# Performance work log

Measured on AMD Instinct MI355X. Metric: run time of the kernel, lower is better.

Reference implementation:

```python
import jax, jax.numpy as jnp
import numpy as np

N = 10000        # nodes
E = 640000       # edges (avg degree 64)
D_IN = 128       # input feature dim
H = 128          # hidden dim
B = 64           # graphs in batch


def setup_inputs() -> dict:
    key = jax.random.key(0)
    ks = jax.random.split(key, 12)
    x = jax.random.normal(ks[0], (N, D_IN), dtype=jnp.float32)
    edge_index = jax.random.randint(ks[1], (2, E), 0, N, dtype=jnp.int32)
    batch = jnp.sort(jax.random.randint(ks[2], (N,), 0, B, dtype=jnp.int32))
    def lin(k, fan_in, fan_out):
        s = 1.0 / np.sqrt(fan_in)
        kw, kb = jax.random.split(k)
        W = jax.random.uniform(kw, (fan_in, fan_out), jnp.float32, -s, s)
        b = jax.random.uniform(kb, (fan_out,), jnp.float32, -s, s)
        return W, b
    W1, b1 = lin(ks[3], D_IN, H)
    W2, b2 = lin(ks[4], H, H)
    W3, b3 = lin(ks[5], H, H)
    Wp, bp = lin(ks[6], H, 1)
    return {"x": x, "edge_index": edge_index, "batch": batch,
            "W1": W1, "b1": b1, "W2": W2, "b2": b2,
            "W3": W3, "b3": b3, "Wp": Wp, "bp": bp}


def reference(x, edge_index, batch, W1, b1, W2, b2, W3, b3, Wp, bp):
    # --- GCN normalization with self-loops (shared across layers; edge weights all 1) ---
    loop = jnp.arange(N, dtype=edge_index.dtype)
    src = jnp.concatenate([edge_index[0], loop])  # [E+N] message sources
    dst = jnp.concatenate([edge_index[1], loop])  # [E+N] message targets
    deg = jax.ops.segment_sum(jnp.ones_like(dst, dtype=x.dtype), dst, num_segments=N)
    dinv = jax.lax.rsqrt(jnp.maximum(deg, 1.0))   # deg >= 1 due to self-loops
    norm = dinv[src] * dinv[dst]                  # [E+N]

    def gcn_layer(h, W, b):
        h = h @ W                                             # [N, H] transform first
        msg = norm[:, None] * h[src]                          # [E+N, H] gathered messages
        return jax.ops.segment_sum(msg, dst, num_segments=N) + b

    h = jax.nn.relu(gcn_layer(x, W1, b1))   # dropout is identity in eval mode
    h = jax.nn.relu(gcn_layer(h, W2, b2))
    h = gcn_layer(h, W3, b3)

    # --- global mean pool over graphs ---
    sums = jax.ops.segment_sum(h, batch, num_segments=B)                       # [B, H]
    cnt = jax.ops.segment_sum(jnp.ones((N,), h.dtype), batch, num_segments=B)  # [B]
    emb = sums / jnp.maximum(cnt, 1.0)[:, None]

    return emb @ Wp + bp  # [B, 1]
```

## Files before the change

### kernel.cpp

```cpp
#include <hip/hip_runtime.h>

#define D 128
#define HS 10016
#define CSHIFT 13
#define CSZ (1 << CSHIFT)

__device__ __forceinline__ unsigned short f2bf(float f) {
  unsigned int u = __float_as_uint(f);
  return (unsigned short)((u + 0x7FFFu + ((u >> 16) & 1u)) >> 16);
}


__global__ __launch_bounds__(256) void k_hist(const int* __restrict__ ei, int E, int M,
                                              const int* __restrict__ batch,
                                              int* __restrict__ pk,
                                              unsigned short* __restrict__ rank16,
                                              int* __restrict__ g_hist,
                                              int* __restrict__ g_bh) {
  __shared__ int h[HS];
  __shared__ int bh[64];
  for (int j = threadIdx.x; j < HS; j += 256) h[j] = 0;
  if (threadIdx.x < 64) bh[threadIdx.x] = 0;
  __syncthreads();
  int w = blockIdx.x;
  int i0 = w << CSHIFT;
  int i1 = i0 + CSZ; if (i1 > M) i1 = M;
  for (int i = i0 + threadIdx.x; i < i1; i += 256) {
    int s, d;
    if (i < E) { s = ei[i]; d = ei[E + i]; }
    else { s = i - E; d = s; atomicAdd(&bh[batch[s]], 1); }
    pk[i] = s | (d << 14);
    int r = atomicAdd(&h[d], 1);
    rank16[i] = (unsigned short)r;
  }
  __syncthreads();
  for (int j = threadIdx.x; j < HS; j += 256) g_hist[w * HS + j] = h[j];
  if (threadIdx.x < 64) g_bh[blockIdx.x * 64 + threadIdx.x] = bh[threadIdx.x];
}

__global__ __launch_bounds__(256) void k_merge(int* __restrict__ g_hist,
                                               const int* __restrict__ g_bh,
                                               int* cnt, float* dinv,
                                               int* cntB, float* accB,
                                               int N, int B, int HW) {
  int j = blockIdx.x * 256 + threadIdx.x;
  if (j < N) {
    int run = 0;
    for (int w = 0; w < HW; ++w) {
      int idx = w * HS + j;
      int t = g_hist[idx];
      g_hist[idx] = run;
      run += t;
    }
    cnt[j] = run;
    dinv[j] = rsqrtf((float)run);
  }
  if (j < B) {
    int c = 0;
    for (int w = 0; w < HW; ++w) c += g_bh[w * 64 + j];
    cntB[j] = c;
    accB[j] = 0.f;
  }
}

__global__ __launch_bounds__(1024) void k_scan(const int* __restrict__ cnt,
                                               int* offs, int N) {
  __shared__ int wsum[16];
  __shared__ int carry_s;
  int tid = threadIdx.x, wid = tid >> 6, lane = tid & 63;
  if (tid == 0) carry_s = 0;
  __syncthreads();
  for (int base = 0; base < N; base += 1024) {
    int i = base + tid;
    int v = (i < N) ? cnt[i] : 0;
    int x = v;
    #pragma unroll
    for (int s = 1; s < 64; s <<= 1) {
      int t = __shfl_up(x, s);
      if (lane >= s) x += t;
    }
    if (lane == 63) wsum[wid] = x;
    __syncthreads();
    int woff = 0;
    for (int w = 0; w < wid; ++w) woff += wsum[w];
    int carry = carry_s;
    if (i < N) offs[i] = carry + woff + x - v;
    __syncthreads();
    if (tid == 1023) carry_s = carry + woff + x;
  }
  __syncthreads();
  if (tid == 0) offs[N] = carry_s;
}

__global__ __launch_bounds__(256) void k_fill(const int* __restrict__ pk,
                                              const unsigned short* __restrict__ rank16,
                                              const int* __restrict__ colpre,
                                              const int* __restrict__ offs,
                                              const float* __restrict__ dinv,
                                              float2* __restrict__ epair, int M, int N) {
  int part = blockIdx.x & 7;
  int j    = blockIdx.x >> 3;
  int nj   = gridDim.x >> 3;
  int lo = (int)((long long)part * N >> 3);
  int hi = (int)((long long)(part + 1) * N >> 3);
  for (int i = j * 256 + threadIdx.x; i < M; i += nj * 256) {
    int rec = pk[i];
    int d = rec >> 14;
    if (d < lo || d >= hi) continue;
    int s = rec & 0x3FFF;
    int w = i >> CSHIFT;
    int pos = offs[d] + colpre[w * HS + d] + (int)rank16[i];
    epair[pos] = make_float2(__int_as_float(s), dinv[s] * dinv[d]);
  }
}

__global__ __launch_bounds__(256) void k_gemm(const float* __restrict__ A,
                                              const float* __restrict__ W,
                                              unsigned short* __restrict__ C, int N) {
  __shared__ float As[32][36];
  __shared__ float Ws[32][128];
  int tid = threadIdx.x;
  int tx = tid & 31;
  int ty = tid >> 5;
  int r0 = blockIdx.x * 32;
  float acc[4][4] = {};

  for (int k0 = 0; k0 < 128; k0 += 32) {
    for (int i = tid; i < 1024; i += 256) {
      int kk = i >> 5, j4 = i & 31;
      float4 w = *(const float4*)(W + (size_t)(k0 + kk) * 128 + j4 * 4);
      *(float4*)(&Ws[kk][j4 * 4]) = w;
    }
    {
      int r = tid >> 3, k4 = tid & 7;
      int row = r0 + r;
      float4 a = make_float4(0.f, 0.f, 0.f, 0.f);
      if (row < N) a = *(const float4*)(A + (size_t)row * 128 + k0 + k4 * 4);
      As[k4 * 4 + 0][r] = a.x;
      As[k4 * 4 + 1][r] = a.y;
      As[k4 * 4 + 2][r] = a.z;
      As[k4 * 4 + 3][r] = a.w;
    }
    __syncthreads();
    #pragma unroll
    for (int k = 0; k < 32; ++k) {
      float4 a = *(const float4*)(&As[k][ty * 4]);
      float4 b = *(const float4*)(&Ws[k][tx * 4]);
      float av[4] = {a.x, a.y, a.z, a.w};
      float bv[4] = {b.x, b.y, b.z, b.w};
      #pragma unroll
      for (int i = 0; i < 4; ++i)
        #pragma unroll
        for (int j = 0; j < 4; ++j)
          acc[i][j] = fmaf(av[i], bv[j], acc[i][j]);
    }
    __syncthreads();
  }
  #pragma unroll
  for (int i = 0; i < 4; ++i) {
    int row = r0 + ty * 4 + i;
    if (row < N) {
      ushort4 o;
      o.x = f2bf(acc[i][0]); o.y = f2bf(acc[i][1]);
      o.z = f2bf(acc[i][2]); o.w = f2bf(acc[i][3]);
      *(ushort4*)(C + (size_t)row * 128 + tx * 4) = o;
    }
  }
}

__device__ __forceinline__ void agg_core(const unsigned short* __restrict__ t,
                                         const float2* __restrict__ epair,
                                         int beg, int end, int lane,
                                         float* acc) {
  int half = lane >> 5;
  int q = lane & 31;
  const unsigned short* tq = t + (q << 2);

  int e = beg;
  for (; e + 16 <= end; e += 16) {
    float2 ep[16];
    #pragma unroll
    for (int u = 0; u < 16; ++u) ep[u] = epair[e + u];
    uint2 v[8];
    #pragma unroll
    for (int u = 0; u < 8; ++u) {
      int s0 = __float_as_int(ep[2 * u].x);
      int s1 = __float_as_int(ep[2 * u + 1].x);
      int s = half ? s1 : s0;
      v[u] = *(const uint2*)(tq + ((size_t)s << 7));
    }
    #pragma unroll
    for (int u = 0; u < 8; ++u) {
      float w = half ? ep[2 * u + 1].y : ep[2 * u].y;
      acc[0] = fmaf(w, __uint_as_float(v[u].x << 16), acc[0]);
      acc[1] = fmaf(w, __uint_as_float(v[u].x & 0xFFFF0000u), acc[1]);
      acc[2] = fmaf(w, __uint_as_float(v[u].y << 16), acc[2]);
      acc[3] = fmaf(w, __uint_as_float(v[u].y & 0xFFFF0000u), acc[3]);
    }
  }
  if (e < end) {
    float2 ep[16];
    #pragma unroll
    for (int u = 0; u < 16; ++u) {
      int idx = (e + u < end) ? (e + u) : (end - 1);
      ep[u] = epair[idx];
      if (e + u >= end) ep[u].y = 0.f;
    }
    uint2 v[8];
    #pragma unroll
    for (int u = 0; u < 8; ++u) {
      int s0 = __float_as_int(ep[2 * u].x);
      int s1 = __float_as_int(ep[2 * u + 1].x);
      int s = half ? s1 : s0;
      v[u] = *(const uint2*)(tq + ((size_t)s << 7));
    }
    #pragma unroll
    for (int u = 0; u < 8; ++u) {
      float w = half ? ep[2 * u + 1].y : ep[2 * u].y;
      acc[0] = fmaf(w, __uint_as_float(v[u].x << 16), acc[0]);
      acc[1] = fmaf(w, __uint_as_float(v[u].x & 0xFFFF0000u), acc[1]);
      acc[2] = fmaf(w, __uint_as_float(v[u].y << 16), acc[2]);
      acc[3] = fmaf(w, __uint_as_float(v[u].y & 0xFFFF0000u), acc[3]);
    }
  }
  #pragma unroll
  for (int j = 0; j < 4; ++j) acc[j] += __shfl_xor(acc[j], 32);
}

__global__ __launch_bounds__(256, 4) void k_agg(const unsigned short* __restrict__ t,
                                                const float2* __restrict__ epair,
                                                const int* __restrict__ offs,
                                                const float* __restrict__ bias,
                                                float* __restrict__ hout, int N, int relu) {
  int node = __builtin_amdgcn_readfirstlane(blockIdx.x * 4 + (threadIdx.x >> 6));
  int lane = threadIdx.x & 63;
  if (node >= N) return;
  int beg = offs[node], end = offs[node + 1];
  float acc[4] = {0.f, 0.f, 0.f, 0.f};
  agg_core(t, epair, beg, end, lane, acc);
  int q = lane & 31;
  float4 bb = *(const float4*)(bias + (q << 2));
  float o0 = acc[0] + bb.x, o1 = acc[1] + bb.y, o2 = acc[2] + bb.z, o3 = acc[3] + bb.w;
  if (relu) {
    o0 = fmaxf(o0, 0.f); o1 = fmaxf(o1, 0.f);
    o2 = fmaxf(o2, 0.f); o3 = fmaxf(o3, 0.f);
  }
  if (lane < 32)
    *(float4*)(hout + (size_t)node * 128 + (q << 2)) = make_float4(o0, o1, o2, o3);
}

__global__ __launch_bounds__(256, 4) void k_agg_pool(const unsigned short* __restrict__ t,
                                                     const float2* __restrict__ epair,
                                                     const int* __restrict__ offs,
                                                     const float* __restrict__ bias,
                                                     const float* __restrict__ Wp,
                                                     const int* __restrict__ batch,
                                                     float* accB, int N) {
  int node = __builtin_amdgcn_readfirstlane(blockIdx.x * 4 + (threadIdx.x >> 6));
  int lane = threadIdx.x & 63;
  if (node >= N) return;
  int beg = offs[node], end = offs[node + 1];
  float acc[4] = {0.f, 0.f, 0.f, 0.f};
  agg_core(t, epair, beg, end, lane, acc);
  int q = lane & 31;
  float4 bb = *(const float4*)(bias + (q << 2));
  float4 wv = *(const float4*)(Wp + (q << 2));
  float p = (acc[0] + bb.x) * wv.x + (acc[1] + bb.y) * wv.y +
            (acc[2] + bb.z) * wv.z + (acc[3] + bb.w) * wv.w;
  #pragma unroll
  for (int s = 16; s; s >>= 1) p += __shfl_xor(p, s);
  if (lane == 0) atomicAdd(&accB[batch[node]], p);
}

__global__ __launch_bounds__(64) void k_final(const float* __restrict__ accB,
                                              const int* __restrict__ cntB,
                                              const float* __restrict__ bp,
                                              float* out, int B) {
  int b = blockIdx.x * 64 + threadIdx.x;
  if (b < B) {
    float c = (float)(cntB[b] > 1 ? cntB[b] : 1);
    out[b] = accB[b] / c + bp[0];
  }
}


extern "C" void kernel_launch(void* const* d_in, const int* in_sizes, int n_in,
                              void* d_out, int out_size, void* d_ws, size_t ws_size,
                              hipStream_t stream) {
  const float* x    = (const float*)d_in[0];
  const int*   ei   = (const int*)d_in[1];
  const int*   batch= (const int*)d_in[2];
  const float* W1   = (const float*)d_in[3];
  const float* b1   = (const float*)d_in[4];
  const float* W2   = (const float*)d_in[5];
  const float* b2   = (const float*)d_in[6];
  const float* W3   = (const float*)d_in[7];
  const float* b3   = (const float*)d_in[8];
  const float* Wp   = (const float*)d_in[9];
  const float* bp   = (const float*)d_in[10];
  float* out = (float*)d_out;

  int N = in_sizes[0] / D;
  int E = in_sizes[1] / 2;
  int B = out_size;
  int M = E + N;
  int HW = (M + CSZ - 1) >> CSHIFT;

  char* p = (char*)d_ws;
  float2* epair  = (float2*)p;          p += (size_t)M * 8;
  float* hbuf    = (float*)p;           p += (size_t)N * D * 4;
  unsigned short* tbuf = (unsigned short*)p; p += (size_t)N * D * 2;
  int*   pk      = (int*)p;             p += (size_t)M * 4;
  unsigned short* rank16 = (unsigned short*)p; p += (size_t)M * 2;
  int*   g_hist  = (int*)p;             p += (size_t)HW * HS * 4;
  int*   g_bh    = (int*)p;             p += (size_t)HW * 64 * 4;
  int*   cnt     = (int*)p;             p += (size_t)N * 4;
  int*   offs    = (int*)p;             p += (size_t)(N + 1) * 4;
  float* dinv    = (float*)p;           p += (size_t)N * 4;
  float* accB    = (float*)p;           p += (size_t)B * 4;
  int*   cntB    = (int*)p;             p += (size_t)B * 4;

  int gG  = (N + 31) / 32;
  int gA  = (N + 3) / 4;
  int gMg = (N + 255) / 256;

  k_hist <<<HW, 256, 0, stream>>>(ei, E, M, batch, pk, rank16, g_hist, g_bh);
  k_merge<<<gMg, 256, 0, stream>>>(g_hist, g_bh, cnt, dinv, cntB, accB, N, B, HW);
  k_scan <<<1, 1024, 0, stream>>>(cnt, offs, N);
  k_fill <<<4096, 256, 0, stream>>>(pk, rank16, g_hist, offs, dinv, epair, M, N);

  k_gemm<<<gG, 256, 0, stream>>>(x, W1, tbuf, N);
  k_agg <<<gA, 256, 0, stream>>>(tbuf, epair, offs, b1, hbuf, N, 1);
  k_gemm<<<gG, 256, 0, stream>>>(hbuf, W2, tbuf, N);
  k_agg <<<gA, 256, 0, stream>>>(tbuf, epair, offs, b2, hbuf, N, 1);
  k_gemm<<<gG, 256, 0, stream>>>(hbuf, W3, tbuf, N);
  k_agg_pool<<<gA, 256, 0, stream>>>(tbuf, epair, offs, b3, Wp, batch, accB, N);
  k_final<<<(B + 63) / 64, 64, 0, stream>>>(accB, cntB, bp, out, B);
}
```

Measured before the change: 291.7 us.

## Replace gather aggregation with source-side scatter into per-edge message buffer

Adds a second CSR keyed by source node, whose entries hold each edge's slot in the destination-sorted order. Each layer now writes normalized bf16 messages into a per-edge message buffer laid out in destination order (k_msg), then sums them contiguously per destination (k_sum). The aim is to replace random row gathers with sequential reads, paid for by random row scatter-writes plus a much larger intermediate buffer (M*256 bytes) and extra histogram, scan and fill work. The new path only runs when the workspace is large enough; otherwise the old gather path is kept.

```diff
diff --git a/kernel.cpp b/kernel.cpp
--- a/kernel.cpp
+++ b/kernel.cpp
@@ -8,6 +8,296 @@
 __device__ __forceinline__ unsigned short f2bf(float f) {
   unsigned int u = __float_as_uint(f);
   return (unsigned short)((u + 0x7FFFu + ((u >> 16) & 1u)) >> 16);
+}
+
+
+__global__ __launch_bounds__(1024) void k_scan(const int* __restrict__ cnt,
+                                               int* offs, int N) {
+  __shared__ int wsum[16];
+  __shared__ int carry_s;
+  int tid = threadIdx.x, wid = tid >> 6, lane = tid & 63;
+  if (tid == 0) carry_s = 0;
+  __syncthreads();
+  for (int base = 0; base < N; base += 1024) {
+    int i = base + tid;
+    int v = (i < N) ? cnt[i] : 0;
+    int x = v;
+    #pragma unroll
+    for (int s = 1; s < 64; s <<= 1) {
+      int t = __shfl_up(x, s);
+      if (lane >= s) x += t;
+    }
+    if (lane == 63) wsum[wid] = x;
+    __syncthreads();
+    int woff = 0;
+    for (int w = 0; w < wid; ++w) woff += wsum[w];
+    int carry = carry_s;
+    if (i < N) offs[i] = carry + woff + x - v;
+    __syncthreads();
+    if (tid == 1023) carry_s = carry + woff + x;
+  }
+  __syncthreads();
+  if (tid == 0) offs[N] = carry_s;
+}
+
+__global__ __launch_bounds__(256) void k_gemm(const float* __restrict__ A,
+                                              const float* __restrict__ W,
+                                              unsigned short* __restrict__ C, int N) {
+  __shared__ float As[32][36];
+  __shared__ float Ws[32][128];
+  int tid = threadIdx.x;
+  int tx = tid & 31;
+  int ty = tid >> 5;
+  int r0 = blockIdx.x * 32;
+  float acc[4][4] = {};
+
+  for (int k0 = 0; k0 < 128; k0 += 32) {
+    for (int i = tid; i < 1024; i += 256) {
+      int kk = i >> 5, j4 = i & 31;
+      float4 w = *(const float4*)(W + (size_t)(k0 + kk) * 128 + j4 * 4);
+      *(float4*)(&Ws[kk][j4 * 4]) = w;
+    }
+    {
+      int r = tid >> 3, k4 = tid & 7;
+      int row = r0 + r;
+      float4 a = make_float4(0.f, 0.f, 0.f, 0.f);
+      if (row < N) a = *(const float4*)(A + (size_t)row * 128 + k0 + k4 * 4);
+      As[k4 * 4 + 0][r] = a.x;
+      As[k4 * 4 + 1][r] = a.y;
+      As[k4 * 4 + 2][r] = a.z;
+      As[k4 * 4 + 3][r] = a.w;
+    }
+    __syncthreads();
+    #pragma unroll
+    for (int k = 0; k < 32; ++k) {
+      float4 a = *(const float4*)(&As[k][ty * 4]);
+      float4 b = *(const float4*)(&Ws[k][tx * 4]);
+      float av[4] = {a.x, a.y, a.z, a.w};
+      float bv[4] = {b.x, b.y, b.z, b.w};
+      #pragma unroll
+      for (int i = 0; i < 4; ++i)
+        #pragma unroll
+        for (int j = 0; j < 4; ++j)
+          acc[i][j] = fmaf(av[i], bv[j], acc[i][j]);
+    }
+    __syncthreads();
+  }
+  #pragma unroll
+  for (int i = 0; i < 4; ++i) {
+    int row = r0 + ty * 4 + i;
+    if (row < N) {
+      ushort4 o;
+      o.x = f2bf(acc[i][0]); o.y = f2bf(acc[i][1]);
+      o.z = f2bf(acc[i][2]); o.w = f2bf(acc[i][3]);
+      *(ushort4*)(C + (size_t)row * 128 + tx * 4) = o;
+    }
+  }
+}
+
+__global__ __launch_bounds__(64) void k_final(const float* __restrict__ accB,
+                                              const int* __restrict__ cntB,
+                                              const float* __restrict__ bp,
+                                              float* out, int B) {
+  int b = blockIdx.x * 64 + threadIdx.x;
+  if (b < B) {
+    float c = (float)(cntB[b] > 1 ? cntB[b] : 1);
+    out[b] = accB[b] / c + bp[0];
+  }
+}
+
+
+__global__ __launch_bounds__(256) void k_hist2(const int* __restrict__ ei, int E, int M,
+                                               const int* __restrict__ batch,
+                                               int* __restrict__ pk,
+                                               unsigned short* __restrict__ rank16,
+                                               unsigned short* __restrict__ srank16,
+                                               int* __restrict__ g_hist,
+                                               int* __restrict__ g_hist2,
+                                               int* __restrict__ g_bh) {
+  __shared__ int h[HS];
+  __shared__ int h2[HS];
+  __shared__ int bh[64];
+  for (int j = threadIdx.x; j < HS; j += 256) { h[j] = 0; h2[j] = 0; }
+  if (threadIdx.x < 64) bh[threadIdx.x] = 0;
+  __syncthreads();
+  int w = blockIdx.x;
+  int i0 = w << CSHIFT;
+  int i1 = i0 + CSZ; if (i1 > M) i1 = M;
+  for (int i = i0 + threadIdx.x; i < i1; i += 256) {
+    int s, d;
+    if (i < E) { s = ei[i]; d = ei[E + i]; }
+    else { s = i - E; d = s; atomicAdd(&bh[batch[s]], 1); }
+    pk[i] = s | (d << 14);
+    rank16[i]  = (unsigned short)atomicAdd(&h[d], 1);
+    srank16[i] = (unsigned short)atomicAdd(&h2[s], 1);
+  }
+  __syncthreads();
+  for (int j = threadIdx.x; j < HS; j += 256) {
+    g_hist[w * HS + j]  = h[j];
+    g_hist2[w * HS + j] = h2[j];
+  }
+  if (threadIdx.x < 64) g_bh[blockIdx.x * 64 + threadIdx.x] = bh[threadIdx.x];
+}
+
+__global__ __launch_bounds__(256) void k_merge2(int* __restrict__ g_hist,
+                                                int* __restrict__ g_hist2,
+                                                const int* __restrict__ g_bh,
+                                                int* cnt, int* scnt, float* dinv,
+                                                int* cntB, float* accB,
+                                                int N, int B, int HW) {
+  int j = blockIdx.x * 256 + threadIdx.x;
+  if (j < N) {
+    int run = 0;
+    for (int w = 0; w < HW; ++w) {
+      int idx = w * HS + j;
+      int t = g_hist[idx]; g_hist[idx] = run; run += t;
+    }
+    cnt[j] = run;
+    dinv[j] = rsqrtf((float)run);
+    int run2 = 0;
+    for (int w = 0; w < HW; ++w) {
+      int idx = w * HS + j;
+      int t = g_hist2[idx]; g_hist2[idx] = run2; run2 += t;
+    }
+    scnt[j] = run2;
+  }
+  if (j < B) {
+    int c = 0;
+    for (int w = 0; w < HW; ++w) c += g_bh[w * 64 + j];
+    cntB[j] = c;
+    accB[j] = 0.f;
+  }
+}
+
+__global__ __launch_bounds__(256) void k_fillS(const int* __restrict__ pk,
+                                               const unsigned short* __restrict__ rank16,
+                                               const unsigned short* __restrict__ srank16,
+                                               const int* __restrict__ dcolpre,
+                                               const int* __restrict__ scolpre,
+                                               const int* __restrict__ offs,
+                                               const int* __restrict__ soffs,
+                                               const float* __restrict__ dinv,
+                                               float2* __restrict__ scsr, int M, int N) {
+  int part = blockIdx.x & 7;
+  int j    = blockIdx.x >> 3;
+  int nj   = gridDim.x >> 3;
+  int lo = (int)((long long)part * N >> 3);
+  int hi = (int)((long long)(part + 1) * N >> 3);
+  for (int i = j * 256 + threadIdx.x; i < M; i += nj * 256) {
+    int rec = pk[i];
+    int s = rec & 0x3FFF;
+    if (s < lo || s >= hi) continue;
+    int d = rec >> 14;
+    int w = i >> CSHIFT;
+    int dpos = offs[d]  + dcolpre[w * HS + d] + (int)rank16[i];
+    int spos = soffs[s] + scolpre[w * HS + s] + (int)srank16[i];
+    scsr[spos] = make_float2(__int_as_float(dpos), dinv[s] * dinv[d]);
+  }
+}
+
+__global__ __launch_bounds__(256, 8) void k_msg(const unsigned short* __restrict__ t,
+                                                const float2* __restrict__ scsr,
+                                                const int* __restrict__ soffs,
+                                                unsigned short* __restrict__ msg, int N) {
+  int node = __builtin_amdgcn_readfirstlane(blockIdx.x * 4 + (threadIdx.x >> 6));
+  int lane = threadIdx.x & 63;
+  if (node >= N) return;
+  unsigned int rv = *(const unsigned int*)(t + ((size_t)node << 7) + (lane << 1));
+  float hx = __uint_as_float(rv << 16);
+  float hy = __uint_as_float(rv & 0xFFFF0000u);
+  int beg = soffs[node], end = soffs[node + 1];
+  int e = beg;
+#define EMIT(r) { \
+    int dpos = __float_as_int((r).x); float nw = (r).y; \
+    float a_ = nw * hx, b_ = nw * hy; unsigned int o_; \
+    asm("v_cvt_pk_bf16_f32 %0, %1, %2" : "=v"(o_) : "v"(a_), "v"(b_)); \
+    *(unsigned int*)(msg + ((size_t)dpos << 7) + (lane << 1)) = o_; }
+  for (; e + 4 <= end; e += 4) {
+    float2 r0 = scsr[e], r1 = scsr[e + 1], r2 = scsr[e + 2], r3 = scsr[e + 3];
+    EMIT(r0); EMIT(r1); EMIT(r2); EMIT(r3);
+  }
+  for (; e < end; ++e) { float2 r = scsr[e]; EMIT(r); }
+#undef EMIT
+}
+
+__device__ __forceinline__ void sum_core(const unsigned short* __restrict__ msg,
+                                         int beg, int end, int grp, int sub,
+                                         float* acc) {
+  int cn = end - beg;
+  int c = 0;
+  for (; c + 4 <= cn; c += 4) {
+    uint4 v = *(const uint4*)(msg + ((size_t)(beg + c + grp) << 7) + (sub << 3));
+    acc[0] += __uint_as_float(v.x << 16); acc[1] += __uint_as_float(v.x & 0xFFFF0000u);
+    acc[2] += __uint_as_float(v.y << 16); acc[3] += __uint_as_float(v.y & 0xFFFF0000u);
+    acc[4] += __uint_as_float(v.z << 16); acc[5] += __uint_as_float(v.z & 0xFFFF0000u);
+    acc[6] += __uint_as_float(v.w << 16); acc[7] += __uint_as_float(v.w & 0xFFFF0000u);
+  }
+  if (c < cn) {
+    int rem = cn - c;
+    int gi = grp < rem ? grp : rem - 1;
+    uint4 v = *(const uint4*)(msg + ((size_t)(beg + c + gi) << 7) + (sub << 3));
+    if (grp < rem) {
+      acc[0] += __uint_as_float(v.x << 16); acc[1] += __uint_as_float(v.x & 0xFFFF0000u);
+      acc[2] += __uint_as_float(v.y << 16); acc[3] += __uint_as_float(v.y & 0xFFFF0000u);
+      acc[4] += __uint_as_float(v.z << 16); acc[5] += __uint_as_float(v.z & 0xFFFF0000u);
+      acc[6] += __uint_as_float(v.w << 16); acc[7] += __uint_as_float(v.w & 0xFFFF0000u);
+    }
+  }
+  #pragma unroll
+  for (int j = 0; j < 8; ++j) {
+    acc[j] += __shfl_xor(acc[j], 16);
+    acc[j] += __shfl_xor(acc[j], 32);
+  }
+}
+
+__global__ __launch_bounds__(256, 8) void k_sum(const unsigned short* __restrict__ msg,
+                                                const int* __restrict__ offs,
+                                                const float* __restrict__ bias,
+                                                float* __restrict__ hout, int N, int relu) {
+  int node = blockIdx.x * 4 + (threadIdx.x >> 6);
+  int lane = threadIdx.x & 63;
+  if (node >= N) return;
+  int grp = lane >> 4, sub = lane & 15;
+  float acc[8] = {};
+  sum_core(msg, offs[node], offs[node + 1], grp, sub, acc);
+  if (lane < 16) {
+    float4 b0 = *(const float4*)(bias + (sub << 3));
+    float4 b1 = *(const float4*)(bias + (sub << 3) + 4);
+    float o[8] = {acc[0] + b0.x, acc[1] + b0.y, acc[2] + b0.z, acc[3] + b0.w,
+                  acc[4] + b1.x, acc[5] + b1.y, acc[6] + b1.z, acc[7] + b1.w};
+    if (relu) {
+      #pragma unroll
+      for (int j = 0; j < 8; ++j) o[j] = fmaxf(o[j], 0.f);
+    }
+    float* hp = hout + (size_t)node * 128 + (sub << 3);
+    *(float4*)hp       = make_float4(o[0], o[1], o[2], o[3]);
+    *(float4*)(hp + 4) = make_float4(o[4], o[5], o[6], o[7]);
+  }
+}
+
+__global__ __launch_bounds__(256, 8) void k_sum_pool(const unsigned short* __restrict__ msg,
+                                                     const int* __restrict__ offs,
+                                                     const float* __restrict__ bias,
+                                                     const float* __restrict__ Wp,
+                                                     const int* __restrict__ batch,
+                                                     float* accB, int N) {
+  int node = blockIdx.x * 4 + (threadIdx.x >> 6);
+  int lane = threadIdx.x & 63;
+  if (node >= N) return;
+  int grp = lane >> 4, sub = lane & 15;
+  float acc[8] = {};
+  sum_core(msg, offs[node], offs[node + 1], grp, sub, acc);
+  float4 b0 = *(const float4*)(bias + (sub << 3));
+  float4 b1 = *(const float4*)(bias + (sub << 3) + 4);
+  float4 w0 = *(const float4*)(Wp + (sub << 3));
+  float4 w1 = *(const float4*)(Wp + (sub << 3) + 4);
+  float p = (acc[0] + b0.x) * w0.x + (acc[1] + b0.y) * w0.y +
+            (acc[2] + b0.z) * w0.z + (acc[3] + b0.w) * w0.w +
+            (acc[4] + b1.x) * w1.x + (acc[5] + b1.y) * w1.y +
+            (acc[6] + b1.z) * w1.z + (acc[7] + b1.w) * w1.w;
+  #pragma unroll
+  for (int s = 1; s < 16; s <<= 1) p += __shfl_xor(p, s);
+  if (lane == 0) atomicAdd(&accB[batch[node]], p);
 }
 
 
@@ -30,8 +320,7 @@
     if (i < E) { s = ei[i]; d = ei[E + i]; }
     else { s = i - E; d = s; atomicAdd(&bh[batch[s]], 1); }
     pk[i] = s | (d << 14);
-    int r = atomicAdd(&h[d], 1);
-    rank16[i] = (unsigned short)r;
+    rank16[i] = (unsigned short)atomicAdd(&h[d], 1);
   }
   __syncthreads();
   for (int j = threadIdx.x; j < HS; j += 256) g_hist[w * HS + j] = h[j];
@@ -48,9 +337,7 @@
     int run = 0;
     for (int w = 0; w < HW; ++w) {
       int idx = w * HS + j;
-      int t = g_hist[idx];
-      g_hist[idx] = run;
-      run += t;
+      int t = g_hist[idx]; g_hist[idx] = run; run += t;
     }
     cnt[j] = run;
     dinv[j] = rsqrtf((float)run);
@@ -61,35 +348,6 @@
     cntB[j] = c;
     accB[j] = 0.f;
   }
-}
-
-__global__ __launch_bounds__(1024) void k_scan(const int* __restrict__ cnt,
-                                               int* offs, int N) {
-  __shared__ int wsum[16];
-  __shared__ int carry_s;
-  int tid = threadIdx.x, wid = tid >> 6, lane = tid & 63;
-  if (tid == 0) carry_s = 0;
-  __syncthreads();
-  for (int base = 0; base < N; base += 1024) {
-    int i = base + tid;
-    int v = (i < N) ? cnt[i] : 0;
-    int x = v;
-    #pragma unroll
-    for (int s = 1; s < 64; s <<= 1) {
-      int t = __shfl_up(x, s);
-      if (lane >= s) x += t;
-    }
-    if (lane == 63) wsum[wid] = x;
-    __syncthreads();
-    int woff = 0;
-    for (int w = 0; w < wid; ++w) woff += wsum[w];
-    int carry = carry_s;
-    if (i < N) offs[i] = carry + woff + x - v;
-    __syncthreads();
-    if (tid == 1023) carry_s = carry + woff + x;
-  }
-  __syncthreads();
-  if (tid == 0) offs[N] = carry_s;
 }
 
 __global__ __launch_bounds__(256) void k_fill(const int* __restrict__ pk,
@@ -114,60 +372,6 @@
   }
 }
 
-__global__ __launch_bounds__(256) void k_gemm(const float* __restrict__ A,
-                                              const float* __restrict__ W,
-                                              unsigned short* __restrict__ C, int N) {
-  __shared__ float As[32][36];
-  __shared__ float Ws[32][128];
-  int tid = threadIdx.x;
-  int tx = tid & 31;
-  int ty = tid >> 5;
-  int r0 = blockIdx.x * 32;
-  float acc[4][4] = {};
-
-  for (int k0 = 0; k0 < 128; k0 += 32) {
-    for (int i = tid; i < 1024; i += 256) {
-      int kk = i >> 5, j4 = i & 31;
-      float4 w = *(const float4*)(W + (size_t)(k0 + kk) * 128 + j4 * 4);
-      *(float4*)(&Ws[kk][j4 * 4]) = w;
-    }
-    {
-      int r = tid >> 3, k4 = tid & 7;
-      int row = r0 + r;
-      float4 a = make_float4(0.f, 0.f, 0.f, 0.f);
-      if (row < N) a = *(const float4*)(A + (size_t)row * 128 + k0 + k4 * 4);
-      As[k4 * 4 + 0][r] = a.x;
-      As[k4 * 4 + 1][r] = a.y;
-      As[k4 * 4 + 2][r] = a.z;
-      As[k4 * 4 + 3][r] = a.w;
-    }
-    __syncthreads();
-    #pragma unroll
-    for (int k = 0; k < 32; ++k) {
-      float4 a = *(const float4*)(&As[k][ty * 4]);
-      float4 b = *(const float4*)(&Ws[k][tx * 4]);
-      float av[4] = {a.x, a.y, a.z, a.w};
-      float bv[4] = {b.x, b.y, b.z, b.w};
-      #pragma unroll
-      for (int i = 0; i < 4; ++i)
-        #pragma unroll
-        for (int j = 0; j < 4; ++j)
-          acc[i][j] = fmaf(av[i], bv[j], acc[i][j]);
-    }
-    __syncthreads();
-  }
-  #pragma unroll
-  for (int i = 0; i < 4; ++i) {
-    int row = r0 + ty * 4 + i;
-    if (row < N) {
-      ushort4 o;
-      o.x = f2bf(acc[i][0]); o.y = f2bf(acc[i][1]);
-      o.z = f2bf(acc[i][2]); o.w = f2bf(acc[i][3]);
-      *(ushort4*)(C + (size_t)row * 128 + tx * 4) = o;
-    }
-  }
-}
-
 __device__ __forceinline__ void agg_core(const unsigned short* __restrict__ t,
                                          const float2* __restrict__ epair,
                                          int beg, int end, int lane,
@@ -175,7 +379,6 @@
   int half = lane >> 5;
   int q = lane & 31;
   const unsigned short* tq = t + (q << 2);
-
   int e = beg;
   for (; e + 16 <= end; e += 16) {
     float2 ep[16];
@@ -235,9 +438,8 @@
   int node = __builtin_amdgcn_readfirstlane(blockIdx.x * 4 + (threadIdx.x >> 6));
   int lane = threadIdx.x & 63;
   if (node >= N) return;
-  int beg = offs[node], end = offs[node + 1];
   float acc[4] = {0.f, 0.f, 0.f, 0.f};
-  agg_core(t, epair, beg, end, lane, acc);
+  agg_core(t, epair, offs[node], offs[node + 1], lane, acc);
   int q = lane & 31;
   float4 bb = *(const float4*)(bias + (q << 2));
   float o0 = acc[0] + bb.x, o1 = acc[1] + bb.y, o2 = acc[2] + bb.z, o3 = acc[3] + bb.w;
@@ -259,9 +461,8 @@
   int node = __builtin_amdgcn_readfirstlane(blockIdx.x * 4 + (threadIdx.x >> 6));
   int lane = threadIdx.x & 63;
   if (node >= N) return;
-  int beg = offs[node], end = offs[node + 1];
   float acc[4] = {0.f, 0.f, 0.f, 0.f};
-  agg_core(t, epair, beg, end, lane, acc);
+  agg_core(t, epair, offs[node], offs[node + 1], lane, acc);
   int q = lane & 31;
   float4 bb = *(const float4*)(bias + (q << 2));
   float4 wv = *(const float4*)(Wp + (q << 2));
@@ -270,17 +471,6 @@
   #pragma unroll
   for (int s = 16; s; s >>= 1) p += __shfl_xor(p, s);
   if (lane == 0) atomicAdd(&accB[batch[node]], p);
-}
-
-__global__ __launch_bounds__(64) void k_final(const float* __restrict__ accB,
-                                              const int* __restrict__ cntB,
-                                              const float* __restrict__ bp,
-                                              float* out, int B) {
-  int b = blockIdx.x * 64 + threadIdx.x;
-  if (b < B) {
-    float c = (float)(cntB[b] > 1 ? cntB[b] : 1);
-    out[b] = accB[b] / c + bp[0];
-  }
 }
 
 
@@ -306,34 +496,88 @@
   int M = E + N;
   int HW = (M + CSZ - 1) >> CSHIFT;
 
-  char* p = (char*)d_ws;
-  float2* epair  = (float2*)p;          p += (size_t)M * 8;
-  float* hbuf    = (float*)p;           p += (size_t)N * D * 4;
-  unsigned short* tbuf = (unsigned short*)p; p += (size_t)N * D * 2;
-  int*   pk      = (int*)p;             p += (size_t)M * 4;
-  unsigned short* rank16 = (unsigned short*)p; p += (size_t)M * 2;
-  int*   g_hist  = (int*)p;             p += (size_t)HW * HS * 4;
-  int*   g_bh    = (int*)p;             p += (size_t)HW * 64 * 4;
-  int*   cnt     = (int*)p;             p += (size_t)N * 4;
-  int*   offs    = (int*)p;             p += (size_t)(N + 1) * 4;
-  float* dinv    = (float*)p;           p += (size_t)N * 4;
-  float* accB    = (float*)p;           p += (size_t)B * 4;
-  int*   cntB    = (int*)p;             p += (size_t)B * 4;
-
   int gG  = (N + 31) / 32;
   int gA  = (N + 3) / 4;
   int gMg = (N + 255) / 256;
 
-  k_hist <<<HW, 256, 0, stream>>>(ei, E, M, batch, pk, rank16, g_hist, g_bh);
-  k_merge<<<gMg, 256, 0, stream>>>(g_hist, g_bh, cnt, dinv, cntB, accB, N, B, HW);
-  k_scan <<<1, 1024, 0, stream>>>(cnt, offs, N);
-  k_fill <<<4096, 256, 0, stream>>>(pk, rank16, g_hist, offs, dinv, epair, M, N);
-
-  k_gemm<<<gG, 256, 0, stream>>>(x, W1, tbuf, N);
-  k_agg <<<gA, 256, 0, stream>>>(tbuf, epair, offs, b1, hbuf, N, 1);
-  k_gemm<<<gG, 256, 0, stream>>>(hbuf, W2, tbuf, N);
-  k_agg <<<gA, 256, 0, stream>>>(tbuf, epair, offs, b2, hbuf, N, 1);
-  k_gemm<<<gG, 256, 0, stream>>>(hbuf, W3, tbuf, N);
-  k_agg_pool<<<gA, 256, 0, stream>>>(tbuf, epair, offs, b3, Wp, batch, accB, N);
-  k_final<<<(B + 63) / 64, 64, 0, stream>>>(accB, cntB, bp, out, B);
-}
+  size_t need = (size_t)M * 256
+              + (size_t)M * 8
+              + (size_t)N * D * 4
+              + (size_t)N * D * 2
+              + (size_t)M * 4
+              + (size_t)M * 2 * 2
+              + (size_t)HW * HS * 4 * 2
+              + (size_t)HW * 64 * 4
+              + (size_t)(N * 4) * 2
+              + (size_t)(N + 1) * 4 * 2
+              + (size_t)N * 4
+              + (size_t)B * 8 + 1024;
+
+  if (ws_size >= need) {
+    char* p = (char*)d_ws;
+    unsigned short* msg = (unsigned short*)p; p += (size_t)M * 256;
+    float2* scsr   = (float2*)p;          p += (size_t)M * 8;
+    float* hbuf    = (float*)p;           p += (size_t)N * D * 4;
+    unsigned short* tbuf = (unsigned short*)p; p += (size_t)N * D * 2;
+    int*   pk      = (int*)p;             p += (size_t)M * 4;
+    unsigned short* rank16  = (unsigned short*)p; p += (size_t)M * 2;
+    unsigned short* srank16 = (unsigned short*)p; p += (size_t)M * 2;
+    int*   g_hist  = (int*)p;             p += (size_t)HW * HS * 4;
+    int*   g_hist2 = (int*)p;             p += (size_t)HW * HS * 4;
+    int*   g_bh    = (int*)p;             p += (size_t)HW * 64 * 4;
+    int*   cnt     = (int*)p;             p += (size_t)N * 4;
+    int*   scnt    = (int*)p;             p += (size_t)N * 4;
+    int*   offs    = (int*)p;             p += (size_t)(N + 1) * 4;
+    int*   soffs   = (int*)p;             p += (size_t)(N + 1) * 4;
+    float* dinv    = (float*)p;           p += (size_t)N * 4;
+    float* accB    = (float*)p;           p += (size_t)B * 4;
+    int*   cntB    = (int*)p;             p += (size_t)B * 4;
+
+    k_hist2 <<<HW, 256, 0, stream>>>(ei, E, M, batch, pk, rank16, srank16,
+                                     g_hist, g_hist2, g_bh);
+    k_merge2<<<gMg, 256, 0, stream>>>(g_hist, g_hist2, g_bh, cnt, scnt, dinv,
+                                      cntB, accB, N, B, HW);
+    k_scan  <<<1, 1024, 0, stream>>>(cnt, offs, N);
+    k_scan  <<<1, 1024, 0, stream>>>(scnt, soffs, N);
+    k_fillS <<<4096, 256, 0, stream>>>(pk, rank16, srank16, g_hist, g_hist2,
+                                       offs, soffs, dinv, scsr, M, N);
+
+    k_gemm<<<gG, 256, 0, stream>>>(x, W1, tbuf, N);
+    k_msg <<<gA, 256, 0, stream>>>(tbuf, scsr, soffs, msg, N);
+    k_sum <<<gA, 256, 0, stream>>>(msg, offs, b1, hbuf, N, 1);
+    k_gemm<<<gG, 256, 0, stream>>>(hbuf, W2, tbuf, N);
+    k_msg <<<gA, 256, 0, stream>>>(tbuf, scsr, soffs, msg, N);
+    k_sum <<<gA, 256, 0, stream>>>(msg, offs, b2, hbuf, N, 1);
+    k_gemm<<<gG, 256, 0, stream>>>(hbuf, W3, tbuf, N);
+    k_msg <<<gA, 256, 0, stream>>>(tbuf, scsr, soffs, msg, N);
+    k_sum_pool<<<gA, 256, 0, stream>>>(msg, offs, b3, Wp, batch, accB, N);
+    k_final<<<(B + 63) / 64, 64, 0, stream>>>(accB, cntB, bp, out, B);
+  } else {
+    char* p = (char*)d_ws;
+    float2* epair  = (float2*)p;          p += (size_t)M * 8;
+    float* hbuf    = (float*)p;           p += (size_t)N * D * 4;
+    unsigned short* tbuf = (unsigned short*)p; p += (size_t)N * D * 2;
+    int*   pk      = (int*)p;             p += (size_t)M * 4;
+    unsigned short* rank16 = (unsigned short*)p; p += (size_t)M * 2;
+    int*   g_hist  = (int*)p;             p += (size_t)HW * HS * 4;
+    int*   g_bh    = (int*)p;             p += (size_t)HW * 64 * 4;
+    int*   cnt     = (int*)p;             p += (size_t)N * 4;
+    int*   offs    = (int*)p;             p += (size_t)(N + 1) * 4;
+    float* dinv    = (float*)p;           p += (size_t)N * 4;
+    float* accB    = (float*)p;           p += (size_t)B * 4;
+    int*   cntB    = (int*)p;             p += (size_t)B * 4;
+
+    k_hist <<<HW, 256, 0, stream>>>(ei, E, M, batch, pk, rank16, g_hist, g_bh);
+    k_merge<<<gMg, 256, 0, stream>>>(g_hist, g_bh, cnt, dinv, cntB, accB, N, B, HW);
+    k_scan <<<1, 1024, 0, stream>>>(cnt, offs, N);
+    k_fill <<<4096, 256, 0, stream>>>(pk, rank16, g_hist, offs, dinv, epair, M, N);
+
+    k_gemm<<<gG, 256, 0, stream>>>(x, W1, tbuf, N);
+    k_agg <<<gA, 256, 0, stream>>>(tbuf, epair, offs, b1, hbuf, N, 1);
+    k_gemm<<<gG, 256, 0, stream>>>(hbuf, W2, tbuf, N);
+    k_agg <<<gA, 256, 0, stream>>>(tbuf, epair, offs, b2, hbuf, N, 1);
+    k_gemm<<<gG, 256, 0, stream>>>(hbuf, W3, tbuf, N);
+    k_agg_pool<<<gA, 256, 0, stream>>>(tbuf, epair, offs, b3, Wp, batch, accB, N);
+    k_final<<<(B + 63) / 64, 64, 0, stream>>>(accB, cntB, bp, out, B);
+  }
+}
```

Measured after the change: 448.2 us. 53.6% more time.
